# Performance work log

Measured on AMD Instinct MI355X. Metric: run time of the kernel, lower is better.

The kernel has to match this reference:

```python
import jax, jax.numpy as jnp
import numpy as np

N_NODES = 10000
N_EDGES = 320000
D_FEAT = 256
N_LAYERS = 4
EPS = 1e-16


def setup_inputs() -> dict:
    key = jax.random.key(0)
    k1, k2, k3 = jax.random.split(key, 3)
    feats = jax.random.normal(k1, (N_NODES, D_FEAT), dtype=jnp.float32)
    src = jax.random.randint(k2, (N_EDGES,), 0, N_NODES, dtype=jnp.int32)
    dst = jax.random.randint(k3, (N_EDGES,), 0, N_NODES, dtype=jnp.int32)
    betas = jnp.ones((N_LAYERS,), dtype=jnp.float32)  # agnn_conv_init_beta = 1.0
    return {"feats": feats, "src": src, "dst": dst, "betas": betas}


def _agnn_layer(h, src, dst, beta, num_nodes):
    # cosine-similarity edge attention (DGL AGNNConv): normalize node feats, dot per edge
    h_norm = h * jax.lax.rsqrt(jnp.sum(h * h, axis=-1, keepdims=True) + EPS)  # [N, d]
    cos = jnp.sum(h_norm[src] * h_norm[dst], axis=-1)                          # [E]
    logits = beta * cos                                                        # [E]
    # edge softmax over incoming edges of each destination node
    m = jax.ops.segment_max(logits, dst, num_segments=num_nodes)               # [N]
    ex = jnp.exp(logits - m[dst])                                              # [E]
    denom = jax.ops.segment_sum(ex, dst, num_segments=num_nodes)               # [N]
    alpha = ex / (denom[dst] + EPS)                                            # [E]
    # scatter-aggregate weighted neighbor features
    msg = alpha[:, None] * h[src]                                              # [E, d]
    return jax.ops.segment_sum(msg, dst, num_segments=num_nodes)               # [N, d]


def reference(feats, src, dst, betas):
    h = feats
    num_nodes = feats.shape[0]
    for i in range(N_LAYERS):
        h = _agnn_layer(h, src, dst, betas[i], num_nodes)
        h = jax.nn.relu(h)
    return h
```

## Files before the change

kernel.cpp:

```cpp
#include <hip/hip_runtime.h>
#include <hip/hip_bf16.h>

#define NN 10000
#define NE 320000
#define D 256
#define D4 64
#define BH 128
#define EPB (NE / BH)


template<int CTRL>
__device__ __forceinline__ float dpp_add(float x) {
    int y = __builtin_amdgcn_update_dpp(0, __float_as_int(x), CTRL, 0xF, 0xF, true);
    return x + __int_as_float(y);
}

__device__ __forceinline__ float wave_red_sum(float x) {
    x = dpp_add<0x111>(x);
    x = dpp_add<0x112>(x);
    x = dpp_add<0x114>(x);
    x = dpp_add<0x118>(x);
    x = dpp_add<0x142>(x);
    x = dpp_add<0x143>(x);
    return __int_as_float(__builtin_amdgcn_readlane(__float_as_int(x), 63));
}

__device__ __forceinline__ float bcast_lane_f(float x, int t) {
    return __int_as_float(__builtin_amdgcn_readlane(__float_as_int(x), t));
}


__global__ void hist_rank_kernel(const int* __restrict__ dst,
                                 int* __restrict__ blockhist, int* __restrict__ rank) {
    __shared__ int lh[NN];
    for (int i = threadIdx.x; i < NN; i += 256) lh[i] = 0;
    __syncthreads();
    int e0 = blockIdx.x * EPB, e1 = e0 + EPB;
    for (int e = e0 + threadIdx.x; e < e1; e += 256)
        rank[e] = atomicAdd(&lh[dst[e]], 1);
    __syncthreads();
    int* bh = blockhist + blockIdx.x * NN;
    for (int i = threadIdx.x; i < NN; i += 256) bh[i] = lh[i];
}

__global__ void colscan_kernel(int* __restrict__ blockhist, int* __restrict__ cnt, int n) {
    int d = blockIdx.x * blockDim.x + threadIdx.x;
    if (d >= n) return;
    int run = 0;
    for (int b = 0; b < BH; ++b) {
        int v = blockhist[b * NN + d];
        blockhist[b * NN + d] = run;
        run += v;
    }
    cnt[d] = run;
}

__global__ void scan_kernel(const int* __restrict__ cnt, int* __restrict__ rowptr, int n) {
    __shared__ int part[256];
    int t = threadIdx.x;
    int chunk = (n + 255) / 256;
    int b = t * chunk;
    int e = b + chunk; if (e > n) e = n;
    int s = 0;
    for (int i = b; i < e; ++i) s += cnt[i];
    part[t] = s;
    __syncthreads();
    for (int off = 1; off < 256; off <<= 1) {
        int v = (t >= off) ? part[t - off] : 0;
        __syncthreads();
        part[t] += v;
        __syncthreads();
    }
    int acc = part[t] - s;
    for (int i = b; i < e; ++i) { rowptr[i] = acc; acc += cnt[i]; }
    if (e == n && b < n) rowptr[n] = acc;
}

__global__ void scatter2_kernel(const int* __restrict__ src, const int* __restrict__ dst,
                                const int* __restrict__ rank, const int* __restrict__ blockhist,
                                const int* __restrict__ rowptr, int* __restrict__ esrc, int nE) {
    int e = blockIdx.x * blockDim.x + threadIdx.x;
    if (e >= nE) return;
    int b = e / EPB;
    int d = dst[e];
    esrc[rowptr[d] + blockhist[b * NN + d] + rank[e]] = src[e];
}


__global__ void norm_kernel(const float4* __restrict__ h, float* __restrict__ inv, int n) {
    int wid  = (blockIdx.x * blockDim.x + threadIdx.x) >> 6;
    int lane = threadIdx.x & 63;
    if (wid >= n) return;
    float4 v = h[wid * D4 + lane];
    float s = wave_red_sum(v.x * v.x + v.y * v.y + v.z * v.z + v.w * v.w);
    if (lane == 0) inv[wid] = rsqrtf(s + 1e-16f);
}


__device__ __forceinline__ float dot4(float4 a, float4 b) {
    return a.x * b.x + a.y * b.y + a.z * b.z + a.w * b.w;
}

__global__ void fused_kernel(const float4* __restrict__ h, const float* __restrict__ inv,
                             float* __restrict__ invN,
                             const int* __restrict__ rowptr, const int* __restrict__ esrc,
                             const float* __restrict__ betas, int layer,
                             float4* __restrict__ out, int n) {
    int wid  = (blockIdx.x * blockDim.x + threadIdx.x) >> 6;
    int lane = threadIdx.x & 63;
    if (wid >= n) return;

    float4 a    = h[wid * D4 + lane];
    float  bivd = betas[layer] * inv[wid];
    int beg = rowptr[wid], end = rowptr[wid + 1];

    float4 acc = make_float4(0.f, 0.f, 0.f, 0.f);
    float dsum = 0.f;

    for (int base = beg; base < end; base += 64) {
        int idx = base + lane;
        int s_l = 0; float iv_l = 0.f;
        if (idx < end) { s_l = esrc[idx]; iv_l = inv[s_l]; }
        int m = end - base; if (m > 64) m = 64;

        int t = 0;
        for (; t + 3 < m; t += 4) {
            int s0 = __builtin_amdgcn_readlane(s_l, t);
            int s1 = __builtin_amdgcn_readlane(s_l, t + 1);
            int s2 = __builtin_amdgcn_readlane(s_l, t + 2);
            int s3 = __builtin_amdgcn_readlane(s_l, t + 3);
            float4 v0 = h[s0 * D4 + lane];
            float4 v1 = h[s1 * D4 + lane];
            float4 v2 = h[s2 * D4 + lane];
            float4 v3 = h[s3 * D4 + lane];
            float i0 = bcast_lane_f(iv_l, t);
            float i1 = bcast_lane_f(iv_l, t + 1);
            float i2 = bcast_lane_f(iv_l, t + 2);
            float i3 = bcast_lane_f(iv_l, t + 3);
            float p0 = wave_red_sum(dot4(a, v0));
            float p1 = wave_red_sum(dot4(a, v1));
            float p2 = wave_red_sum(dot4(a, v2));
            float p3 = wave_red_sum(dot4(a, v3));
            float e0 = __expf(p0 * bivd * i0);
            float e1 = __expf(p1 * bivd * i1);
            float e2 = __expf(p2 * bivd * i2);
            float e3 = __expf(p3 * bivd * i3);
            dsum += (e0 + e1) + (e2 + e3);
            acc.x += e0 * v0.x + e1 * v1.x + e2 * v2.x + e3 * v3.x;
            acc.y += e0 * v0.y + e1 * v1.y + e2 * v2.y + e3 * v3.y;
            acc.z += e0 * v0.z + e1 * v1.z + e2 * v2.z + e3 * v3.z;
            acc.w += e0 * v0.w + e1 * v1.w + e2 * v2.w + e3 * v3.w;
        }
        for (; t < m; ++t) {
            int   s0 = __builtin_amdgcn_readlane(s_l, t);
            float i0 = bcast_lane_f(iv_l, t);
            float4 v0 = h[s0 * D4 + lane];
            float p0 = wave_red_sum(dot4(a, v0));
            float e0 = __expf(p0 * bivd * i0);
            dsum += e0;
            acc.x += e0 * v0.x; acc.y += e0 * v0.y;
            acc.z += e0 * v0.z; acc.w += e0 * v0.w;
        }
    }

    float r = 1.f / (dsum + 1e-16f);
    float4 w2;
    w2.x = fmaxf(acc.x * r, 0.f); w2.y = fmaxf(acc.y * r, 0.f);
    w2.z = fmaxf(acc.z * r, 0.f); w2.w = fmaxf(acc.w * r, 0.f);
    out[wid * D4 + lane] = w2;

    float s = wave_red_sum(dot4(w2, w2));
    if (lane == 0) invN[wid] = rsqrtf(s + 1e-16f);
}


extern "C" void kernel_launch(void* const* d_in, const int* in_sizes, int n_in,
                              void* d_out, int out_size, void* d_ws, size_t ws_size,
                              hipStream_t stream) {
    const float* feats = (const float*)d_in[0];
    const int*   src   = (const int*)d_in[1];
    const int*   dst   = (const int*)d_in[2];
    const float* betas = (const float*)d_in[3];
    float* out = (float*)d_out;

    float* hA        = (float*)d_ws;
    float* hB        = hA + NN * D;
    float* inv0      = hB + NN * D;
    float* inv1      = inv0 + NN;
    int*   rowptr    = (int*)(inv1 + NN);
    int*   cnt       = rowptr + (NN + 1);
    int*   esrc      = cnt + NN;
    int*   rank      = esrc + NE;
    int*   blockhist = rank + NE;

    hist_rank_kernel<<<BH, 256, 0, stream>>>(dst, blockhist, rank);
    colscan_kernel<<<(NN + 255) / 256, 256, 0, stream>>>(blockhist, cnt, NN);
    scan_kernel<<<1, 256, 0, stream>>>(cnt, rowptr, NN);
    scatter2_kernel<<<(NE + 255) / 256, 256, 0, stream>>>(src, dst, rank, blockhist,
                                                          rowptr, esrc, NE);

    norm_kernel<<<(NN * 64 + 255) / 256, 256, 0, stream>>>((const float4*)feats, inv0, NN);

    const int node_blocks = (NN * 64 + 255) / 256;

    const float* hin = feats;
    float* invCur = inv0;
    float* invNxt = inv1;
    for (int l = 0; l < 4; ++l) {
        float* hout = (l == 3) ? out : ((l & 1) ? hB : hA);
        fused_kernel<<<node_blocks, 256, 0, stream>>>((const float4*)hin, invCur, invNxt,
                                                      rowptr, esrc, betas, l,
                                                      (float4*)hout, NN);
        hin = hout;
        float* tmp = invCur; invCur = invNxt; invNxt = tmp;
    }
}
```

Before: 191.9 us.

## Store normalized features in fp16 and split aggregation into edge chunks with reduction

Node features are now kept as fp16 normalized vectors plus a per-node norm, which halves gather traffic, and cosine similarity becomes a plain dot product. Aggregation is split into 16-edge chunks, one wave per chunk, to balance load across nodes with different degrees. A second kernel reduces the chunk partials and writes the next layer's normalized fp16 features. The costs are reduced precision, the skipped max-subtraction in the softmax (safe only because cos is bounded), extra launches, and partial-sum traffic.

```diff
diff --git a/kernel.cpp b/kernel.cpp
--- a/kernel.cpp
+++ b/kernel.cpp
@@ -1,12 +1,13 @@
 #include <hip/hip_runtime.h>
-#include <hip/hip_bf16.h>
+#include <hip/hip_fp16.h>
 
 #define NN 10000
 #define NE 320000
 #define D 256
-#define D4 64
 #define BH 128
 #define EPB (NE / BH)
+#define CSZ 16
+#define MAXCH 30000
 
 
 template<int CTRL>
@@ -25,8 +26,24 @@
     return __int_as_float(__builtin_amdgcn_readlane(__float_as_int(x), 63));
 }
 
-__device__ __forceinline__ float bcast_lane_f(float x, int t) {
+__device__ __forceinline__ float rl_f(float x, int t) {
     return __int_as_float(__builtin_amdgcn_readlane(__float_as_int(x), t));
+}
+
+union H2U { __half2 h; unsigned u; };
+
+__device__ __forceinline__ float4 unpack4(uint2 r) {
+    H2U a, b; a.u = r.x; b.u = r.y;
+    float2 f01 = __half22float2(a.h);
+    float2 f23 = __half22float2(b.h);
+    return make_float4(f01.x, f01.y, f23.x, f23.y);
+}
+
+__device__ __forceinline__ uint2 pack4(float4 v) {
+    H2U a, b;
+    a.h = __floats2half2_rn(v.x, v.y);
+    b.h = __floats2half2_rn(v.z, v.w);
+    return make_uint2(a.u, b.u);
 }
 
 
@@ -55,7 +72,7 @@
     cnt[d] = run;
 }
 
-__global__ void scan_kernel(const int* __restrict__ cnt, int* __restrict__ rowptr, int n) {
+__global__ void scan_kernel(const int* __restrict__ cnt, int* __restrict__ ofs, int n) {
     __shared__ int part[256];
     int t = threadIdx.x;
     int chunk = (n + 255) / 256;
@@ -72,8 +89,8 @@
         __syncthreads();
     }
     int acc = part[t] - s;
-    for (int i = b; i < e; ++i) { rowptr[i] = acc; acc += cnt[i]; }
-    if (e == n && b < n) rowptr[n] = acc;
+    for (int i = b; i < e; ++i) { ofs[i] = acc; acc += cnt[i]; }
+    if (e == n && b < n) ofs[n] = acc;
 }
 
 __global__ void scatter2_kernel(const int* __restrict__ src, const int* __restrict__ dst,
@@ -86,91 +103,148 @@
     esrc[rowptr[d] + blockhist[b * NN + d] + rank[e]] = src[e];
 }
 
-
-__global__ void norm_kernel(const float4* __restrict__ h, float* __restrict__ inv, int n) {
+__global__ void nchunk_kernel(const int* __restrict__ rowptr, int* __restrict__ nchunk, int n) {
+    int d = blockIdx.x * blockDim.x + threadIdx.x;
+    if (d >= n) return;
+    int deg = rowptr[d + 1] - rowptr[d];
+    nchunk[d] = (deg + CSZ - 1) / CSZ;
+}
+
+__global__ void fillchunk_kernel(const int* __restrict__ chunkofs, int* __restrict__ chunk_node, int n) {
+    int d = blockIdx.x * blockDim.x + threadIdx.x;
+    if (d >= n) return;
+    int b = chunkofs[d], e = chunkofs[d + 1];
+    for (int j = b; j < e; ++j) chunk_node[j] = d;
+}
+
+
+__global__ void norm_kernel(const float4* __restrict__ h, uint2* __restrict__ hn,
+                            float* __restrict__ nrm, int n) {
     int wid  = (blockIdx.x * blockDim.x + threadIdx.x) >> 6;
     int lane = threadIdx.x & 63;
     if (wid >= n) return;
-    float4 v = h[wid * D4 + lane];
-    float s = wave_red_sum(v.x * v.x + v.y * v.y + v.z * v.z + v.w * v.w);
-    if (lane == 0) inv[wid] = rsqrtf(s + 1e-16f);
-}
-
-
-__device__ __forceinline__ float dot4(float4 a, float4 b) {
-    return a.x * b.x + a.y * b.y + a.z * b.z + a.w * b.w;
-}
-
-__global__ void fused_kernel(const float4* __restrict__ h, const float* __restrict__ inv,
-                             float* __restrict__ invN,
-                             const int* __restrict__ rowptr, const int* __restrict__ esrc,
-                             const float* __restrict__ betas, int layer,
-                             float4* __restrict__ out, int n) {
-    int wid  = (blockIdx.x * blockDim.x + threadIdx.x) >> 6;
+    float4 v = h[wid * 64 + lane];
+    float tot = wave_red_sum(v.x * v.x + v.y * v.y + v.z * v.z + v.w * v.w);
+    float rs = rsqrtf(tot + 1e-16f);
+    hn[wid * 64 + lane] = pack4(make_float4(v.x * rs, v.y * rs, v.z * rs, v.w * rs));
+    if (lane == 0) nrm[wid] = 1.0f / rs;
+}
+
+
+__global__ __launch_bounds__(256, 8)
+void phase1_kernel(const uint2* __restrict__ hnin, const float* __restrict__ nrmin,
+                   const int* __restrict__ rowptr, const int* __restrict__ chunkofs,
+                   const int* __restrict__ chunk_node, const int* __restrict__ esrc,
+                   const float* __restrict__ betas, int layer,
+                   float4* __restrict__ pacc, float* __restrict__ pdsum) {
+    int w    = (blockIdx.x * blockDim.x + threadIdx.x) >> 6;
     int lane = threadIdx.x & 63;
-    if (wid >= n) return;
-
-    float4 a    = h[wid * D4 + lane];
-    float  bivd = betas[layer] * inv[wid];
-    int beg = rowptr[wid], end = rowptr[wid + 1];
+    int tot  = chunkofs[NN];
+    if (w >= tot) return;
+
+    int node = chunk_node[w];
+    int rb   = rowptr[node];
+    int j    = w - chunkofs[node];
+    int cbeg = rb + j * CSZ;
+    int cend = rowptr[node + 1];
+    if (cend > cbeg + CSZ) cend = cbeg + CSZ;
+    int m = cend - cbeg;
+
+    float4 a = unpack4(hnin[node * 64 + lane]);
+    float beta = betas[layer];
+
+    int s_l = 0; float nm_l = 0.f;
+    if (lane < m) { s_l = esrc[cbeg + lane]; nm_l = nrmin[s_l]; }
 
     float4 acc = make_float4(0.f, 0.f, 0.f, 0.f);
     float dsum = 0.f;
 
-    for (int base = beg; base < end; base += 64) {
-        int idx = base + lane;
-        int s_l = 0; float iv_l = 0.f;
-        if (idx < end) { s_l = esrc[idx]; iv_l = inv[s_l]; }
-        int m = end - base; if (m > 64) m = 64;
-
-        int t = 0;
-        for (; t + 3 < m; t += 4) {
-            int s0 = __builtin_amdgcn_readlane(s_l, t);
-            int s1 = __builtin_amdgcn_readlane(s_l, t + 1);
-            int s2 = __builtin_amdgcn_readlane(s_l, t + 2);
-            int s3 = __builtin_amdgcn_readlane(s_l, t + 3);
-            float4 v0 = h[s0 * D4 + lane];
-            float4 v1 = h[s1 * D4 + lane];
-            float4 v2 = h[s2 * D4 + lane];
-            float4 v3 = h[s3 * D4 + lane];
-            float i0 = bcast_lane_f(iv_l, t);
-            float i1 = bcast_lane_f(iv_l, t + 1);
-            float i2 = bcast_lane_f(iv_l, t + 2);
-            float i3 = bcast_lane_f(iv_l, t + 3);
-            float p0 = wave_red_sum(dot4(a, v0));
-            float p1 = wave_red_sum(dot4(a, v1));
-            float p2 = wave_red_sum(dot4(a, v2));
-            float p3 = wave_red_sum(dot4(a, v3));
-            float e0 = __expf(p0 * bivd * i0);
-            float e1 = __expf(p1 * bivd * i1);
-            float e2 = __expf(p2 * bivd * i2);
-            float e3 = __expf(p3 * bivd * i3);
-            dsum += (e0 + e1) + (e2 + e3);
-            acc.x += e0 * v0.x + e1 * v1.x + e2 * v2.x + e3 * v3.x;
-            acc.y += e0 * v0.y + e1 * v1.y + e2 * v2.y + e3 * v3.y;
-            acc.z += e0 * v0.z + e1 * v1.z + e2 * v2.z + e3 * v3.z;
-            acc.w += e0 * v0.w + e1 * v1.w + e2 * v2.w + e3 * v3.w;
+    int nf = m & ~3;
+    uint2 b0, b1, b2, b3;
+    if (nf > 0) {
+        b0 = hnin[__builtin_amdgcn_readlane(s_l, 0) * 64 + lane];
+        b1 = hnin[__builtin_amdgcn_readlane(s_l, 1) * 64 + lane];
+        b2 = hnin[__builtin_amdgcn_readlane(s_l, 2) * 64 + lane];
+        b3 = hnin[__builtin_amdgcn_readlane(s_l, 3) * 64 + lane];
+    }
+    for (int g = 0; g < nf; g += 4) {
+        float4 v0 = unpack4(b0);
+        float4 v1 = unpack4(b1);
+        float4 v2 = unpack4(b2);
+        float4 v3 = unpack4(b3);
+        float n0 = rl_f(nm_l, g),     n1 = rl_f(nm_l, g + 1);
+        float n2 = rl_f(nm_l, g + 2), n3 = rl_f(nm_l, g + 3);
+        int gn = g + 4;
+        if (gn < nf) {
+            b0 = hnin[__builtin_amdgcn_readlane(s_l, gn)     * 64 + lane];
+            b1 = hnin[__builtin_amdgcn_readlane(s_l, gn + 1) * 64 + lane];
+            b2 = hnin[__builtin_amdgcn_readlane(s_l, gn + 2) * 64 + lane];
+            b3 = hnin[__builtin_amdgcn_readlane(s_l, gn + 3) * 64 + lane];
         }
-        for (; t < m; ++t) {
-            int   s0 = __builtin_amdgcn_readlane(s_l, t);
-            float i0 = bcast_lane_f(iv_l, t);
-            float4 v0 = h[s0 * D4 + lane];
-            float p0 = wave_red_sum(dot4(a, v0));
-            float e0 = __expf(p0 * bivd * i0);
-            dsum += e0;
-            acc.x += e0 * v0.x; acc.y += e0 * v0.y;
-            acc.z += e0 * v0.z; acc.w += e0 * v0.w;
-        }
+        float p0 = a.x * v0.x + a.y * v0.y + a.z * v0.z + a.w * v0.w;
+        float p1 = a.x * v1.x + a.y * v1.y + a.z * v1.z + a.w * v1.w;
+        float p2 = a.x * v2.x + a.y * v2.y + a.z * v2.z + a.w * v2.w;
+        float p3 = a.x * v3.x + a.y * v3.y + a.z * v3.z + a.w * v3.w;
+        p0 = wave_red_sum(p0); p1 = wave_red_sum(p1);
+        p2 = wave_red_sum(p2); p3 = wave_red_sum(p3);
+        float e0 = __expf(beta * p0);
+        float e1 = __expf(beta * p1);
+        float e2 = __expf(beta * p2);
+        float e3 = __expf(beta * p3);
+        dsum += (e0 + e1) + (e2 + e3);
+        float w0 = e0 * n0, w1 = e1 * n1, w2 = e2 * n2, w3 = e3 * n3;
+        acc.x += w0 * v0.x + w1 * v1.x + w2 * v2.x + w3 * v3.x;
+        acc.y += w0 * v0.y + w1 * v1.y + w2 * v2.y + w3 * v3.y;
+        acc.z += w0 * v0.z + w1 * v1.z + w2 * v2.z + w3 * v3.z;
+        acc.w += w0 * v0.w + w1 * v1.w + w2 * v2.w + w3 * v3.w;
+    }
+    for (int t = nf; t < m; ++t) {
+        float4 v0 = unpack4(hnin[__builtin_amdgcn_readlane(s_l, t) * 64 + lane]);
+        float n0 = rl_f(nm_l, t);
+        float p0 = a.x * v0.x + a.y * v0.y + a.z * v0.z + a.w * v0.w;
+        p0 = wave_red_sum(p0);
+        float e0 = __expf(beta * p0);
+        dsum += e0;
+        float w0 = e0 * n0;
+        acc.x += w0 * v0.x; acc.y += w0 * v0.y;
+        acc.z += w0 * v0.z; acc.w += w0 * v0.w;
+    }
+
+    pacc[w * 64 + lane] = acc;
+    if (lane == 0) pdsum[w] = dsum;
+}
+
+
+__global__ void phase2_kernel(const int* __restrict__ chunkofs,
+                              const float4* __restrict__ pacc, const float* __restrict__ pdsum,
+                              float4* __restrict__ outf, uint2* __restrict__ hnout,
+                              float* __restrict__ nrmout, int lastLayer, int n) {
+    int node = (blockIdx.x * blockDim.x + threadIdx.x) >> 6;
+    int lane = threadIdx.x & 63;
+    if (node >= n) return;
+    int cb = chunkofs[node], ce = chunkofs[node + 1];
+
+    float4 acc = make_float4(0.f, 0.f, 0.f, 0.f);
+    float dsum = 0.f;
+    for (int c = cb; c < ce; ++c) {
+        float4 p = pacc[c * 64 + lane];
+        acc.x += p.x; acc.y += p.y; acc.z += p.z; acc.w += p.w;
+        dsum += pdsum[c];
     }
 
     float r = 1.f / (dsum + 1e-16f);
-    float4 w2;
-    w2.x = fmaxf(acc.x * r, 0.f); w2.y = fmaxf(acc.y * r, 0.f);
-    w2.z = fmaxf(acc.z * r, 0.f); w2.w = fmaxf(acc.w * r, 0.f);
-    out[wid * D4 + lane] = w2;
-
-    float s = wave_red_sum(dot4(w2, w2));
-    if (lane == 0) invN[wid] = rsqrtf(s + 1e-16f);
+    float4 w;
+    w.x = fmaxf(acc.x * r, 0.f); w.y = fmaxf(acc.y * r, 0.f);
+    w.z = fmaxf(acc.z * r, 0.f); w.w = fmaxf(acc.w * r, 0.f);
+
+    if (lastLayer) {
+        outf[node * 64 + lane] = w;
+    } else {
+        float ss = wave_red_sum(w.x * w.x + w.y * w.y + w.z * w.z + w.w * w.w);
+        float rs = rsqrtf(ss + 1e-16f);
+        hnout[node * 64 + lane] = pack4(make_float4(w.x * rs, w.y * rs, w.z * rs, w.w * rs));
+        if (lane == 0) nrmout[node] = 1.0f / rs;
+    }
 }
 
 
@@ -183,15 +257,20 @@
     const float* betas = (const float*)d_in[3];
     float* out = (float*)d_out;
 
-    float* hA        = (float*)d_ws;
-    float* hB        = hA + NN * D;
-    float* inv0      = hB + NN * D;
-    float* inv1      = inv0 + NN;
-    int*   rowptr    = (int*)(inv1 + NN);
-    int*   cnt       = rowptr + (NN + 1);
-    int*   esrc      = cnt + NN;
-    int*   rank      = esrc + NE;
-    int*   blockhist = rank + NE;
+    float4* pacc      = (float4*)d_ws;
+    uint2*  hn0       = (uint2*)(pacc + MAXCH * 64);
+    uint2*  hn1       = hn0 + NN * 64;
+    float*  pdsum     = (float*)(hn1 + NN * 64);
+    float*  nrm0      = pdsum + MAXCH;
+    float*  nrm1      = nrm0 + NN;
+    int*    rowptr    = (int*)(nrm1 + NN);
+    int*    cnt       = rowptr + (NN + 1);
+    int*    nchunk    = cnt + NN;
+    int*    chunkofs  = nchunk + NN;
+    int*    chunk_node= chunkofs + (NN + 1);
+    int*    esrc      = chunk_node + MAXCH;
+    int*    rank      = esrc + NE;
+    int*    blockhist = rank + NE;
 
     hist_rank_kernel<<<BH, 256, 0, stream>>>(dst, blockhist, rank);
     colscan_kernel<<<(NN + 255) / 256, 256, 0, stream>>>(blockhist, cnt, NN);
@@ -199,19 +278,28 @@
     scatter2_kernel<<<(NE + 255) / 256, 256, 0, stream>>>(src, dst, rank, blockhist,
                                                           rowptr, esrc, NE);
 
-    norm_kernel<<<(NN * 64 + 255) / 256, 256, 0, stream>>>((const float4*)feats, inv0, NN);
-
-    const int node_blocks = (NN * 64 + 255) / 256;
-
-    const float* hin = feats;
-    float* invCur = inv0;
-    float* invNxt = inv1;
+    nchunk_kernel<<<(NN + 255) / 256, 256, 0, stream>>>(rowptr, nchunk, NN);
+    scan_kernel<<<1, 256, 0, stream>>>(nchunk, chunkofs, NN);
+    fillchunk_kernel<<<(NN + 255) / 256, 256, 0, stream>>>(chunkofs, chunk_node, NN);
+
+    norm_kernel<<<(NN * 64 + 255) / 256, 256, 0, stream>>>((const float4*)feats,
+                                                           hn0, nrm0, NN);
+
+    const int p1_blocks = MAXCH / 4;
+    const int p2_blocks = (NN + 3) / 4;
+
+    const uint2* hnin  = hn0;
+    const float* nrmin = nrm0;
     for (int l = 0; l < 4; ++l) {
-        float* hout = (l == 3) ? out : ((l & 1) ? hB : hA);
-        fused_kernel<<<node_blocks, 256, 0, stream>>>((const float4*)hin, invCur, invNxt,
-                                                      rowptr, esrc, betas, l,
-                                                      (float4*)hout, NN);
-        hin = hout;
-        float* tmp = invCur; invCur = invNxt; invNxt = tmp;
-    }
-}
+        uint2* hnout  = (l & 1) ? hn0 : hn1;
+        float* nrmout = (l & 1) ? nrm0 : nrm1;
+        phase1_kernel<<<p1_blocks, 256, 0, stream>>>(hnin, nrmin, rowptr, chunkofs,
+                                                     chunk_node, esrc, betas, l,
+                                                     pacc, pdsum);
+        phase2_kernel<<<p2_blocks, 256, 0, stream>>>(chunkofs, pacc, pdsum,
+                                                     (float4*)out, hnout, nrmout,
+                                                     (l == 3) ? 1 : 0, NN);
+        hnin  = hnout;
+        nrmin = nrmout;
+    }
+}
```

Result: slower. 201.3 us (+4.9%).
